# Kernel optimization log

Hardware: AMD Instinct MI355X
Metric: run time of the kernel (lower is better)

## Reference

```python
import jax, jax.numpy as jnp
import numpy as np
from jax import lax

DIM = 512; HEADS = 8; HD = DIM // HEADS; SM = 16; NS = 3
B = 8; HH = 32; WW = 32; N = HH * WW; HL = DIM // 4


def setup_inputs() -> dict:
    key = jax.random.key(0)
    ks = iter(jax.random.split(key, 64))
    def g(shape, s=0.02):
        return jax.random.normal(next(ks), shape, dtype=jnp.float32) * s
    z = lambda *sh: jnp.zeros(sh, jnp.float32)
    inp = {
        'x': jax.random.normal(next(ks), (B, N, DIM), dtype=jnp.float32),
        'H': HH, 'W': WW,
        'qkv_w': g((NS, 3 * DIM, DIM)),
        'proj_w': g((DIM, DIM)), 'proj_b': z(DIM),
        'pos_sw': g((HEADS, SM, HD, 2)), 'neg_sw': g((HEADS, SM, HD, 2)),
        'spec_mix': jnp.ones((HEADS, SM), jnp.float32),
        'ca_w1': g((DIM // 2, DIM)), 'ca_b1': z(DIM // 2),
        'ca_w2': g((HEADS * 4, DIM // 2)), 'ca_b2': z(HEADS * 4),
        'lstm_wih_f': g((4 * HL, DIM)), 'lstm_whh_f': g((4 * HL, HL)),
        'lstm_bih_f': z(4 * HL), 'lstm_bhh_f': z(4 * HL),
        'lstm_wih_b': g((4 * HL, DIM)), 'lstm_whh_b': g((4 * HL, HL)),
        'lstm_bih_b': z(4 * HL), 'lstm_bhh_b': z(4 * HL),
        'mha_in_w': g((3 * DIM, DIM)), 'mha_in_b': z(3 * DIM),
        'mha_out_w': g((DIM, DIM)), 'mha_out_b': z(DIM),
        'ge_w1': g((DIM // 2, DIM)), 'ge_b1': z(DIM // 2),
        'ge_w2': g((HEADS * 2, DIM // 2)), 'ge_b2': z(HEADS * 2),
        'spw': jnp.ones((NS, HEADS, HD), jnp.float32),
        'dwc_w5': g((HD, 1, 5, 5), 0.05), 'dwc_b5': z(HD),
        'dwc_w7': g((HD, 1, 7, 7), 0.05), 'dwc_b7': z(HD),
        'dwc_w9': g((HD, 1, 9, 9), 0.05), 'dwc_b9': z(HD),
        'mode_w': jnp.ones((3,), jnp.float32) / 3.0,
    }
    return inp


def reference(x, H, W, qkv_w, proj_w, proj_b, pos_sw, neg_sw, spec_mix,
              ca_w1, ca_b1, ca_w2, ca_b2,
              lstm_wih_f, lstm_whh_f, lstm_bih_f, lstm_bhh_f,
              lstm_wih_b, lstm_whh_b, lstm_bih_b, lstm_bhh_b,
              mha_in_w, mha_in_b, mha_out_w, mha_out_b,
              ge_w1, ge_b1, ge_w2, ge_b2, spw,
              dwc_w5, dwc_b5, dwc_w7, dwc_b7, dwc_w9, dwc_b9, mode_w):
    Bn, Nn, C = x.shape
    heads = HEADS; hd = C // heads

    # ---------- DynamicContextEncoder ----------
    def lstm_dir(xs, wih, whh, bih, bhh):
        # xs: (N, B, C); PyTorch gate order i,f,g,o
        gates_x = xs @ wih.T + (bih + bhh)
        hdim = whh.shape[1]
        def step(carry, gx):
            h, c = carry
            gi = gx + h @ whh.T
            i, f, gg, o = jnp.split(gi, 4, axis=-1)
            c = jax.nn.sigmoid(f) * c + jax.nn.sigmoid(i) * jnp.tanh(gg)
            h = jax.nn.sigmoid(o) * jnp.tanh(c)
            return (h, c), h
        z0 = jnp.zeros((xs.shape[1], hdim), xs.dtype)
        _, hs = lax.scan(step, (z0, z0), gates_x)
        return hs

    xs = jnp.swapaxes(x, 0, 1)  # (N, B, C)
    h_f = lstm_dir(xs, lstm_wih_f, lstm_whh_f, lstm_bih_f, lstm_bhh_f)
    h_b = lstm_dir(xs[::-1], lstm_wih_b, lstm_whh_b, lstm_bih_b, lstm_bhh_b)[::-1]
    local_ctx = jnp.concatenate([h_f, h_b], -1).mean(0)  # (B, dim//2)
    local_ctx = jnp.pad(local_ctx, ((0, 0), (0, C - local_ctx.shape[1])))

    nh2 = heads // 2; hd2 = C // nh2
    qkv_c = x @ mha_in_w.T + mha_in_b
    qc, kc, vc = jnp.split(qkv_c, 3, -1)
    sh = lambda t: t.reshape(Bn, Nn, nh2, hd2).transpose(0, 2, 1, 3)
    qc, kc, vc = sh(qc), sh(kc), sh(vc)
    attn = jax.nn.softmax(jnp.einsum('bhnd,bhmd->bhnm', qc, kc) / float(np.sqrt(hd2)), -1)
    ac = jnp.einsum('bhnm,bhmd->bhnd', attn, vc).transpose(0, 2, 1, 3).reshape(Bn, Nn, C)
    ac = ac @ mha_out_w.T + mha_out_b
    combined = x.mean(1) + local_ctx + ac.mean(1)
    coeffs = jax.nn.sigmoid(jax.nn.relu(combined @ ca_w1.T + ca_b1) @ ca_w2.T + ca_b2)
    coeffs = coeffs.reshape(Bn, heads, 4)

    # ---------- GradientInformedMixer coefficients (x_grad is zeros) ----------
    gz = jnp.zeros((Bn, C), x.dtype)
    gmix = jax.nn.softmax((jnp.tanh(gz @ ge_w1.T + ge_b1) @ ge_w2.T + ge_b2).reshape(Bn, heads, 2), -1)

    # ---------- SpectralPolarityMixer ----------
    smix = jax.nn.softmax(spec_mix, -1).mean(-1)[None, :, None, None]  # per-head scalar
    wp = (pos_sw[..., 0] + 1j * pos_sw[..., 1])[:, :SM, :SM]
    wn = (neg_sw[..., 0] + 1j * neg_sw[..., 1])[:, :SM, :SM]

    def spectral(t):
        tf = jnp.fft.rfft2(t)[:, :, :SM, :SM]
        tp = jnp.fft.irfft2(tf * wp[None], s=(Nn, hd))
        tn = jnp.fft.irfft2(tf * wn[None], s=(Nn, hd))
        return tp + tn * smix

    def safe_pow(t, p):  # relu(t)**p with safe grads
        tp = jnp.where(t > 0, t, 1.0)
        return jnp.where(t > 0, tp ** p, 0.0)

    mw = jax.nn.softmax(mode_w, 0)
    def dwc(xi, w, b):
        return lax.conv_general_dilated(xi, w, (1, 1), 'SAME',
                                        feature_group_count=xi.shape[1],
                                        dimension_numbers=('NCHW', 'OIHW', 'NCHW')) + b[None, :, None, None]

    c0, c1, c2, c3 = [coeffs[:, :, i][:, :, None, None] for i in range(4)]
    g0, g1 = gmix[:, :, 0][:, :, None, None], gmix[:, :, 1][:, :, None, None]

    outs = []
    for s in range(NS):
        qkv = (x @ qkv_w[s].T).reshape(Bn, Nn, 3, heads, hd).transpose(2, 0, 3, 1, 4)
        q, k, v = qkv[0], qkv[1], qkv[2]  # (B, heads, N, hd)
        q = spectral(q); k = spectral(k)
        p = (1.0 + jnp.abs(spw[s]))[None, :, None, :]
        q_pos = safe_pow(q, p); q_neg = safe_pow(-q, p)
        k_pos = safe_pow(k, p); k_neg = safe_pow(-k, p)
        kvpp = jnp.einsum('bhnd,bhne->bhde', k_pos, v)
        kvnn = jnp.einsum('bhnd,bhne->bhde', k_neg, v)
        z = (jnp.einsum('bhnd,bhd->bhn', q_pos, k_pos.sum(2))
             + jnp.einsum('bhnd,bhd->bhn', q_neg, k_neg.sum(2)) + 1e-6)[..., None]
        same = (c0 * jnp.einsum('bhnd,bhde->bhne', q_pos, kvpp)
                + c1 * jnp.einsum('bhnd,bhde->bhne', q_neg, kvnn)) / z
        opp = (c2 * jnp.einsum('bhnd,bhde->bhne', q_pos, kvnn)
               + c3 * jnp.einsum('bhnd,bhde->bhne', q_neg, kvpp)) / z
        mixed = g0 * same + g1 * opp
        v_img = v.reshape(Bn * heads, H, W, hd).transpose(0, 3, 1, 2)
        vcv = mw[0] * dwc(v_img, dwc_w5, dwc_b5) + mw[1] * dwc(v_img, dwc_w7, dwc_b7) + mw[2] * dwc(v_img, dwc_w9, dwc_b9)
        vcv = vcv.transpose(0, 2, 3, 1).reshape(Bn, heads, Nn, hd)
        outs.append(mixed + vcv)

    out = jnp.stack(outs).mean(0).transpose(0, 2, 1, 3).reshape(Bn, Nn, C)
    return out @ proj_w.T + proj_b
```

## Files before the change

kernel.cpp:

```cpp
#include <hip/hip_runtime.h>
#include <hip/hip_bf16.h>
#include <math.h>

typedef __bf16 bf16x8 __attribute__((ext_vector_type(8)));
typedef __bf16 bf16x4 __attribute__((ext_vector_type(4)));
typedef float  f32x4  __attribute__((ext_vector_type(4)));
typedef const float __attribute__((address_space(1)))* gf1p;

#define MFMA(a,b,c) __builtin_amdgcn_mfma_f32_16x16x32_bf16(a, b, c, 0, 0, 0)
#define LOG2E 1.4426950408889634f

static constexpr size_t OFF_R0    = 0;
static constexpr size_t OFF_GXT   = 12582912;
static constexpr size_t OFF_ACCUM = OFF_GXT;
static constexpr size_t OFF_FINAL = OFF_GXT + 4194304;
static constexpr size_t SOFF      = OFF_GXT + 8388608;
static constexpr size_t OFF_ROWSUM= SOFF;
static constexpr size_t OFF_ACMP  = OFF_ROWSUM;
static constexpr size_t OFF_COLW  = OFF_ROWSUM + 32768;
static constexpr size_t OFF_BM    = OFF_COLW;
static constexpr size_t OFF_XPART = OFF_COLW + 327680;
static constexpr size_t OFF_ACM   = OFF_COLW + 524288;
static constexpr size_t OFF_XMEAN = OFF_ACM + 4096;
static constexpr size_t OFF_LC    = OFF_XMEAN + 4096;
static constexpr size_t OFF_COEF  = OFF_LC + 2048;
static constexpr size_t OFF_GMIX  = OFF_COEF + 256;
static constexpr size_t OFF_MW    = OFF_GMIX + 16;
static constexpr size_t OFF_CONV9 = OFF_MW + 4;
static constexpr size_t OFF_CBIAS = OFF_CONV9 + 5184;
static constexpr size_t OFF_WEFF  = OFF_CBIAS + 64;
static constexpr size_t OFF_PPOW  = OFF_WEFF + 4096;
static constexpr size_t OFF_LBIAS = OFF_PPOW + 1536;
static constexpr size_t OFF_W2    = OFF_LBIAS + 1024;
static constexpr size_t OFF_W1CS  = OFF_W2 + 2048;
static constexpr size_t OFF_W1T   = OFF_W1CS + 16384;
static constexpr size_t OFF_XB    = OFF_FINAL;
static constexpr size_t OFF_QW    = OFF_FINAL + 2097152;
static constexpr size_t OFF_MW2   = OFF_FINAL + 3276800;
static constexpr size_t OFF_WFB   = OFF_FINAL + 3670016;
static constexpr size_t OFF_WBB   = OFF_FINAL + 3801088;
static constexpr size_t OFF_PWB   = OFF_FINAL + 3932160;

__device__ __forceinline__ float sigm(float x){ return __builtin_amdgcn_rcpf(1.0f + exp2f(-LOG2E*x)); }
__device__ __forceinline__ float tanhx(float x){ return 2.0f*__builtin_amdgcn_rcpf(1.0f + exp2f(-2.0f*LOG2E*x)) - 1.0f; }
__device__ __forceinline__ unsigned pk2(float a, float b){
  union { __bf16 h[2]; unsigned u; } z; z.h[0]=(__bf16)a; z.h[1]=(__bf16)b; return z.u;
}
__device__ __forceinline__ unsigned pk2b(__bf16 a, __bf16 b){
  union { __bf16 h[2]; unsigned u; } z; z.h[0]=a; z.h[1]=b; return z.u;
}
__device__ __forceinline__ void powpair(float t, float p, float& pos, float& neg){
  float a = fabsf(t);
  float v = (a > 0.f) ? exp2f(p * __log2f(a)) : 0.f;
  pos = (t > 0.f) ? v : 0.f;
  neg = (t < 0.f) ? v : 0.f;
}
__device__ __forceinline__ f32x4 fz4(){ return (f32x4){0.f,0.f,0.f,0.f}; }

__global__ void k_cvt_all(const float* __restrict__ x, const float* __restrict__ qkv_w,
                          const float* __restrict__ mha_in_w, const float* __restrict__ wih_f,
                          const float* __restrict__ wih_b, const float* __restrict__ proj_w,
                          float* __restrict__ ws){
  int b = blockIdx.x;
  const float* src; __bf16* dst; int base;
  if (b < 2048){      src=x;        dst=(__bf16*)(ws+OFF_XB);  base=b; }
  else if (b < 3200){ src=qkv_w;    dst=(__bf16*)(ws+OFF_QW);  base=b-2048; }
  else if (b < 3584){ src=mha_in_w; dst=(__bf16*)(ws+OFF_MW2); base=b-3200; }
  else if (b < 3712){ src=wih_f;    dst=(__bf16*)(ws+OFF_WFB); base=b-3584; }
  else if (b < 3840){ src=wih_b;    dst=(__bf16*)(ws+OFF_WBB); base=b-3712; }
  else {              src=proj_w;   dst=(__bf16*)(ws+OFF_PWB); base=b-3840; }
  int i = (base*256 + threadIdx.x)*8;
  f32x4 u0 = *(const f32x4*)(src+i), u1 = *(const f32x4*)(src+i+4);
  bf16x8 v;
  #pragma unroll
  for (int j=0;j<4;++j){ v[j]=(__bf16)u0[j]; v[j+4]=(__bf16)u1[j]; }
  *(bf16x8*)(dst+i) = v;
}

__global__ void k_const(const float* __restrict__ ge_b1, const float* __restrict__ ge_w2,
                        const float* __restrict__ ge_b2, const float* __restrict__ mode_w,
                        const float* __restrict__ w5, const float* __restrict__ b5,
                        const float* __restrict__ w7, const float* __restrict__ b7,
                        const float* __restrict__ w9, const float* __restrict__ b9,
                        const float* __restrict__ pos_sw, const float* __restrict__ neg_sw,
                        const float* __restrict__ spw,
                        const float* __restrict__ bih_f, const float* __restrict__ bhh_f,
                        const float* __restrict__ bih_b, const float* __restrict__ bhh_b,
                        float* __restrict__ ws){
  int tid = threadIdx.x;
  __shared__ float mw[3];
  __shared__ float tgh[256];
  __shared__ float sbuf[16];
  tgh[tid] = tanhf(ge_b1[tid]);
  if (tid == 0){
    float m0=mode_w[0], m1=mode_w[1], m2=mode_w[2];
    float mx = fmaxf(m0, fmaxf(m1,m2));
    float e0=expf(m0-mx), e1=expf(m1-mx), e2=expf(m2-mx);
    float s = e0+e1+e2;
    mw[0]=e0/s; mw[1]=e1/s; mw[2]=e2/s;
    ws[OFF_MW+0]=mw[0]; ws[OFF_MW+1]=mw[1]; ws[OFF_MW+2]=mw[2];
  }
  __syncthreads();
  if (tid < 16){
    float s = ge_b2[tid];
    for (int i=0;i<256;++i) s += ge_w2[tid*256+i]*tgh[i];
    sbuf[tid] = s;
  }
  __syncthreads();
  if (tid < 8){
    float a = sbuf[2*tid], b = sbuf[2*tid+1];
    float m = fmaxf(a,b);
    float ea = expf(a-m), eb = expf(b-m);
    ws[OFF_GMIX+2*tid]   = ea/(ea+eb);
    ws[OFF_GMIX+2*tid+1] = eb/(ea+eb);
  }
  for (int j=tid;j<512;j+=256){
    ws[OFF_LBIAS+j]     = bih_f[j]+bhh_f[j];
    ws[OFF_LBIAS+512+j] = bih_b[j]+bhh_b[j];
  }
  for (int f=tid; f<5184; f+=256){
    int d=f/81, t=f%81, ky=t/9, kx=t%9, dy=ky-4, dx=kx-4;
    float v = mw[2]*w9[d*81+t];
    if (dy>=-3 && dy<=3 && dx>=-3 && dx<=3) v += mw[1]*w7[d*49 + (dy+3)*7 + (dx+3)];
    if (dy>=-2 && dy<=2 && dx>=-2 && dx<=2) v += mw[0]*w5[d*25 + (dy+2)*5 + (dx+2)];
    ws[OFF_CONV9+f] = v;
  }
  if (tid<64) ws[OFF_CBIAS+tid] = mw[0]*b5[tid]+mw[1]*b7[tid]+mw[2]*b9[tid];
  for (int f=tid; f<2048; f+=256){
    int h=f>>8, k1=(f>>4)&15, k2=f&15;
    int src = ((h*16+k1)*64 + k2)*2;
    ws[OFF_WEFF+2*f]   = pos_sw[src]   + 0.0625f*neg_sw[src];
    ws[OFF_WEFF+2*f+1] = pos_sw[src+1] + 0.0625f*neg_sw[src+1];
  }
  for (int f=tid; f<1536; f+=256) ws[OFF_PPOW+f] = 1.0f + fabsf(spw[f]);
  for (int f=tid; f<1024; f+=256){
    int e=f>>4, k2=f&15; int ph=(e*k2)&63;
    float th = (float)ph * (6.283185307179586f/64.0f);
    ws[OFF_W2+2*f]   = cosf(th);
    ws[OFF_W2+2*f+1] = -sinf(th);
  }
  __bf16* w1cs = (__bf16*)(ws + OFF_W1CS);
  for (int f=tid; f<32768; f+=256){
    int r=f>>10, m=f&1023; int k1=r&15; int ph=(k1*m)&1023;
    float th = (float)ph * (6.283185307179586f/1024.0f);
    w1cs[f] = (__bf16)((r<16)?cosf(th):-sinf(th));
  }
  __bf16* w1t = (__bf16*)(ws + OFF_W1T);
  for (int f=tid; f<32768; f+=256){
    int n=f>>5, r=f&31; int k1=r&15; int ph=(k1*n)&1023;
    float th = (float)ph * (6.283185307179586f/1024.0f);
    w1t[f] = (__bf16)((r<16)?cosf(th):sinf(th));
  }
}

template<typename CT>
__global__ __launch_bounds__(256,2) void k_gemm_bf(const __bf16* __restrict__ A, const __bf16* __restrict__ W,
                                                   const float* __restrict__ bias, CT* __restrict__ C,
                                                   int NB_N, int N, int K){
  __shared__ __bf16 As[128][40];
  __shared__ __bf16 Ws[128][40];
  int tid = threadIdx.x;
  int nwg = gridDim.x, o = blockIdx.x;
  int cpx = nwg >> 3;
  int wg = (o & 7)*cpx + (o >> 3);
  int n0 = (wg % NB_N) * 128, m0 = (wg / NB_N) * 128;
  int l = tid & 63, wid = tid >> 6, lr = l & 15, lg = l >> 4;
  int wr = wid >> 1, wc = wid & 1;
  f32x4 acc[4][4];
  #pragma unroll
  for (int i=0;i<4;++i){ acc[i][0]=fz4(); acc[i][1]=fz4(); acc[i][2]=fz4(); acc[i][3]=fz4(); }
  int srow = tid >> 1, sk = (tid & 1) * 16;
  const __bf16* Ap = A + (size_t)(m0 + srow) * K + sk;
  const __bf16* Wp = W + (size_t)(n0 + srow) * K + sk;
  for (int k0 = 0; k0 < K; k0 += 32){
    bf16x8 a0 = *(const bf16x8*)(Ap), a1 = *(const bf16x8*)(Ap+8);
    bf16x8 w0 = *(const bf16x8*)(Wp), w1 = *(const bf16x8*)(Wp+8);
    Ap += 32; Wp += 32;
    __syncthreads();
    *(bf16x8*)&As[srow][sk]   = a0;  *(bf16x8*)&As[srow][sk+8] = a1;
    *(bf16x8*)&Ws[srow][sk]   = w0;  *(bf16x8*)&Ws[srow][sk+8] = w1;
    __syncthreads();
    bf16x8 aF[4], bF[4];
    #pragma unroll
    for (int mf=0;mf<4;++mf) aF[mf] = *(const bf16x8*)&As[wr*64+mf*16+lr][lg*8];
    #pragma unroll
    for (int nf=0;nf<4;++nf) bF[nf] = *(const bf16x8*)&Ws[wc*64+nf*16+lr][lg*8];
    #pragma unroll
    for (int mf=0;mf<4;++mf)
      #pragma unroll
      for (int nf=0;nf<4;++nf) acc[mf][nf] = MFMA(aF[mf], bF[nf], acc[mf][nf]);
  }
  #pragma unroll
  for (int mf=0;mf<4;++mf)
    #pragma unroll
    for (int nf=0;nf<4;++nf){
      int row = m0 + wr*64 + mf*16 + lg*4;
      int col = n0 + wc*64 + nf*16 + lr;
      float bv = bias ? bias[col] : 0.f;
      #pragma unroll
      for (int r=0;r<4;++r) C[(size_t)(row+r)*N + col] = (CT)(acc[mf][nf][r] + bv);
    }
}

__global__ __launch_bounds__(256,2) void k_gemm_acc(const float* __restrict__ accum, const __bf16* __restrict__ W,
                                                    const float* __restrict__ bias, float* __restrict__ C){
  const int N = 512, K = 512, NB_N = 4;
  __shared__ __bf16 As[128][40];
  __shared__ __bf16 Ws[128][40];
  int tid = threadIdx.x;
  int nwg = gridDim.x, o = blockIdx.x;
  int cpx = nwg >> 3;
  int wg = (o & 7)*cpx + (o >> 3);
  int n0 = (wg % NB_N) * 128, m0 = (wg / NB_N) * 128;
  int l = tid & 63, wid = tid >> 6, lr = l & 15, lg = l >> 4;
  int wr = wid >> 1, wc = wid & 1;
  f32x4 acc[4][4];
  #pragma unroll
  for (int i=0;i<4;++i){ acc[i][0]=fz4(); acc[i][1]=fz4(); acc[i][2]=fz4(); acc[i][3]=fz4(); }
  int srow = tid >> 1, sk = (tid & 1) * 16;
  int row = m0 + srow;
  int bb = row >> 10, nn = row & 1023;
  const float* Abase = accum + ((size_t)bb*8192 + nn)*64;
  const __bf16* Wp = W + (size_t)(n0 + srow) * K + sk;
  const float s3 = 1.0f/3.0f;
  for (int k0 = 0; k0 < K; k0 += 32){
    int c0 = k0 + sk;
    const float* Ap = Abase + (size_t)(c0>>6)*65536 + (c0&63);
    f32x4 a0=*(const f32x4*)(Ap), a1=*(const f32x4*)(Ap+4), a2=*(const f32x4*)(Ap+8), a3=*(const f32x4*)(Ap+12);
    bf16x8 w0 = *(const bf16x8*)(Wp), w1 = *(const bf16x8*)(Wp+8);
    Wp += 32;
    __syncthreads();
    bf16x8 va, vb;
    #pragma unroll
    for (int j=0;j<4;++j){ va[j]=(__bf16)(a0[j]*s3); va[j+4]=(__bf16)(a1[j]*s3);
                           vb[j]=(__bf16)(a2[j]*s3); vb[j+4]=(__bf16)(a3[j]*s3); }
    *(bf16x8*)&As[srow][sk]   = va;  *(bf16x8*)&As[srow][sk+8] = vb;
    *(bf16x8*)&Ws[srow][sk]   = w0;  *(bf16x8*)&Ws[srow][sk+8] = w1;
    __syncthreads();
    bf16x8 aF[4], bF[4];
    #pragma unroll
    for (int mf=0;mf<4;++mf) aF[mf] = *(const bf16x8*)&As[wr*64+mf*16+lr][lg*8];
    #pragma unroll
    for (int nf=0;nf<4;++nf) bF[nf] = *(const bf16x8*)&Ws[wc*64+nf*16+lr][lg*8];
    #pragma unroll
    for (int mf=0;mf<4;++mf)
      #pragma unroll
      for (int nf=0;nf<4;++nf) acc[mf][nf] = MFMA(aF[mf], bF[nf], acc[mf][nf]);
  }
  #pragma unroll
  for (int mf=0;mf<4;++mf)
    #pragma unroll
    for (int nf=0;nf<4;++nf){
      int orow = m0 + wr*64 + mf*16 + lg*4;
      int col = n0 + wc*64 + nf*16 + lr;
      float bv = bias[col];
      #pragma unroll
      for (int r=0;r<4;++r) C[(size_t)(orow+r)*N + col] = acc[mf][nf][r] + bv;
    }
}

__global__ __launch_bounds__(256,1) void k_lstm_scan(const float* __restrict__ whh_f,
                                                     const float* __restrict__ whh_b,
                                                     const float* __restrict__ gates,
                                                     float* __restrict__ lc){
  int dir = blockIdx.x >> 3, b = blockIdx.x & 7;
  const float* __restrict__ whh = dir ? whh_b : whh_f;
  const float* gx0 = gates + (size_t)b*1048576;
  gf1p gx1 = (gf1p)(unsigned long long)gx0;
  int tid=threadIdx.x, w=tid>>6, l=tid&63;
  int lr=l&15, lg=l>>4;
  bf16x8 wf[4][2][4];
  #pragma unroll
  for (int q=0;q<4;++q)
    #pragma unroll
    for (int t=0;t<2;++t)
      #pragma unroll
      for (int kc=0;kc<4;++kc){
        const float* p = whh + (size_t)(q*128 + w*32 + t*16 + lr)*128 + kc*32 + lg*8;
        bf16x8 v;
        #pragma unroll
        for (int j=0;j<8;++j) v[j]=(__bf16)p[j];
        wf[q][t][kc]=v;
      }
  __shared__ __bf16 hbuf[2][132];
  for (int i=tid; i<264; i+=256) ((__bf16*)hbuf)[i] = (__bf16)0.0f;
  int tsel = l&1, rsel = (l>>1)&3;
  int hrow = w*32 + tsel*16 + lg*4 + rsel;
  long toff = (dir ? (long)1023*1024 : 0) + dir*512 + hrow;
  long tstride = dir ? -1024 : 1024;
  float cs=0.f, hs=0.f;
  float g0[4], g1[4], g2[4], g3[4];
  #pragma unroll
  for (int q=0;q<4;++q) g0[q] = gx1[toff + q*128];
  toff += tstride;
  #pragma unroll
  for (int q=0;q<4;++q) g1[q] = gx1[toff + q*128];
  toff += tstride;
  #pragma unroll
  for (int q=0;q<4;++q) g2[q] = gx1[toff + q*128];
  toff += tstride;
  #pragma unroll
  for (int q=0;q<4;++q) g3[q] = gx1[toff + q*128];
  toff += tstride;
  __syncthreads();

#define LSTM_STEP(RB, WB, G) { \
    float gq[4]; \
    _Pragma("unroll") for (int q=0;q<4;++q) gq[q]=G[q]; \
    _Pragma("unroll") for (int q=0;q<4;++q) G[q] = gx1[toff + q*128]; \
    toff += tstride; \
    if (toff < 0) toff = 0;   \
    bf16x8 hf[4]; \
    _Pragma("unroll") for (int kc=0;kc<4;++kc) hf[kc] = *(const bf16x8*)&hbuf[RB][kc*32 + lg*8]; \
    f32x4 acc[4][2]; \
    _Pragma("unroll") for (int q=0;q<4;++q){ acc[q][0]=fz4(); acc[q][1]=fz4(); } \
    _Pragma("unroll") for (int kc=0;kc<4;++kc) \
      _Pragma("unroll") for (int q=0;q<4;++q){ \
        acc[q][0] = MFMA(wf[q][0][kc], hf[kc], acc[q][0]); \
        acc[q][1] = MFMA(wf[q][1][kc], hf[kc], acc[q][1]); } \
    float gv[4]; \
    _Pragma("unroll") for (int q=0;q<4;++q){ \
      f32x4 v0 = acc[q][0], v1 = acc[q][1]; \
      float a01 = (rsel&1) ? v0[1] : v0[0]; \
      float a23 = (rsel&1) ? v0[3] : v0[2]; \
      float av  = (rsel&2) ? a23 : a01; \
      float b01 = (rsel&1) ? v1[1] : v1[0]; \
      float b23 = (rsel&1) ? v1[3] : v1[2]; \
      float bv  = (rsel&2) ? b23 : b01; \
      gv[q] = (tsel ? bv : av) + gq[q]; } \
    float ii=sigm(gv[0]), ff=sigm(gv[1]), gg=tanhx(gv[2]), oo=sigm(gv[3]); \
    cs = ff*cs + ii*gg; \
    float hv = oo*tanhx(cs); \
    hs += hv; \
    if (!(l&8)) hbuf[WB][hrow] = (__bf16)hv; \
    asm volatile("s_waitcnt lgkmcnt(0)" ::: "memory"); \
    __builtin_amdgcn_sched_barrier(0); \
    __builtin_amdgcn_s_barrier(); \
    __builtin_amdgcn_sched_barrier(0); }

  for (int it=0; it<256; ++it){
    LSTM_STEP(0, 1, g0)
    LSTM_STEP(1, 0, g1)
    LSTM_STEP(0, 1, g2)
    LSTM_STEP(1, 0, g3)
  }
#undef LSTM_STEP
  if (!(l&8)) lc[b*256 + dir*128 + hrow] = hs*(1.f/1024.f);
}

template<int MODE>
__global__ __launch_bounds__(256,1) void k_mha(const __bf16* __restrict__ qkv, float* __restrict__ rowsum,
                                               float* __restrict__ colw){
  int rb = blockIdx.x, h2 = blockIdx.y, b = blockIdx.z;
  __shared__ __bf16 Qs[256][136];
  __shared__ __bf16 Ks[128][136];
  int tid=threadIdx.x, l=tid&63, w=tid>>6, lr=l&15, lg=l>>4;
  {
    const float qs = LOG2E / sqrtf(128.0f);
    int row = tid;
    const __bf16* p = qkv + ((size_t)(b*1024 + rb*256 + row))*1536 + h2*128;
    #pragma unroll
    for (int cc=0; cc<128; cc+=8){
      bf16x8 u = *(const bf16x8*)(p+cc);
      bf16x8 v;
      #pragma unroll
      for (int j=0;j<8;++j) v[j]=(__bf16)((float)u[j]*qs);
      *(bf16x8*)&Qs[row][cc] = v;
    }
  }
  float rs[4][4];
  if (MODE==1){
    #pragma unroll
    for (int mf=0;mf<4;++mf){ rs[mf][0]=0.f; rs[mf][1]=0.f; rs[mf][2]=0.f; rs[mf][3]=0.f; }
  } else {
    #pragma unroll
    for (int mf=0;mf<4;++mf)
      #pragma unroll
      for (int r=0;r<4;++r)
        rs[mf][r] = 1.0f / rowsum[((size_t)(b*4+h2))*1024 + rb*256 + w*64 + mf*16 + lg*4 + r];
  }
  for (int mc=0; mc<8; ++mc){
    __syncthreads();
    {
      int row = tid>>1, co = (tid&1)*64;
      const __bf16* p = qkv + ((size_t)(b*1024 + mc*128 + row))*1536 + 512 + h2*128 + co;
      #pragma unroll
      for (int cc=0; cc<64; cc+=8)
        *(bf16x8*)&Ks[row][co+cc] = *(const bf16x8*)(p+cc);
    }
    __syncthreads();
    f32x4 acc[4][8];
    #pragma unroll
    for (int mf=0;mf<4;++mf)
      #pragma unroll
      for (int nf=0;nf<8;++nf) acc[mf][nf]=fz4();
    #pragma unroll
    for (int ks=0;ks<4;++ks){
      bf16x8 aF[4], bFv[8];
      #pragma unroll
      for (int mf=0;mf<4;++mf) aF[mf] = *(const bf16x8*)&Qs[w*64+mf*16+lr][ks*32+lg*8];
      #pragma unroll
      for (int nf=0;nf<8;++nf) bFv[nf] = *(const bf16x8*)&Ks[nf*16+lr][ks*32+lg*8];
      #pragma unroll
      for (int mf=0;mf<4;++mf)
        #pragma unroll
        for (int nf=0;nf<8;++nf) acc[mf][nf] = MFMA(aF[mf], bFv[nf], acc[mf][nf]);
    }
    if (MODE==1){
      #pragma unroll
      for (int mf=0;mf<4;++mf)
        #pragma unroll
        for (int nf=0;nf<8;++nf)
          #pragma unroll
          for (int r=0;r<4;++r) rs[mf][r] += exp2f(acc[mf][nf][r]);
    } else {
      #pragma unroll
      for (int nf=0;nf<8;++nf){
        float cv = 0.f;
        #pragma unroll
        for (int mf=0;mf<4;++mf)
          #pragma unroll
          for (int r=0;r<4;++r) cv += exp2f(acc[mf][nf][r])*rs[mf][r];
        cv += __shfl_xor(cv,16);
        cv += __shfl_xor(cv,32);
        if (lg==0)
          colw[(((size_t)(rb*4+w)*8 + b)*4 + h2)*1024 + mc*128 + nf*16 + lr] = cv;
      }
    }
  }
  if (MODE==1){
    #pragma unroll
    for (int mf=0;mf<4;++mf)
      #pragma unroll
      for (int r=0;r<4;++r){
        float v = rs[mf][r];
        v += __shfl_xor(v,1); v += __shfl_xor(v,2); v += __shfl_xor(v,4); v += __shfl_xor(v,8);
        if (lr==0) rowsum[((size_t)(b*4+h2))*1024 + rb*256 + w*64 + mf*16 + lg*4 + r] = v;
      }
  }
}

__global__ void k_mha3(const __bf16* __restrict__ qkv, const float* __restrict__ colw, float* __restrict__ acmp){
  int h2 = blockIdx.x, b = blockIdx.y, ms = blockIdx.z;
  int tid = threadIdx.x;
  __shared__ float cwred[128];
  if (tid < 128){
    float cw=0.f;
    #pragma unroll
    for (int t16=0;t16<16;++t16) cw += colw[(((size_t)t16*8 + b)*4 + h2)*1024 + ms*128 + tid];
    cwred[tid]=cw;
  }
  __syncthreads();
  int e = tid & 127, half = tid >> 7;
  float s = 0.f;
  for (int ml = half*64; ml < half*64+64; ++ml)
    s += cwred[ml] * (float)qkv[((size_t)(b*1024 + ms*128 + ml))*1536 + 1024 + h2*128 + e];
  __shared__ float red[256];
  red[tid]=s; __syncthreads();
  if (tid<128) acmp[((size_t)(ms*8+b))*512 + h2*128 + e] = red[tid]+red[tid+128];
}

__global__ void k_xmean1(const float* __restrict__ x, float* __restrict__ xpart){
  int sl = blockIdx.x, b = blockIdx.y;
  int tid = threadIdx.x;
  #pragma unroll
  for (int cc=0; cc<2; ++cc){
    int c = tid + cc*256;
    float s=0.f;
    for (int n=sl*64; n<sl*64+64; ++n) s += x[((size_t)(b*1024+n))*512 + c];
    xpart[((size_t)(b*16+sl))*512 + c] = s;
  }
}

__global__ __launch_bounds__(256) void k_coeffs(float* __restrict__ ws,
                        const float* __restrict__ mow, const float* __restrict__ mob,
                        const float* __restrict__ ca_w1, const float* __restrict__ ca_b1,
                        const float* __restrict__ ca_w2, const float* __restrict__ ca_b2){
  int b = blockIdx.x, tid = threadIdx.x;
  __shared__ float av[512], comb[512], hid[256];
  for (int i=tid;i<512;i+=256){
    float s = 0.f;
    #pragma unroll
    for (int ms=0; ms<8; ++ms) s += ws[OFF_ACMP + ((size_t)(ms*8+b))*512 + i];
    av[i] = s*(1.f/1024.f);
  }
  __syncthreads();
  for (int c=tid;c<512;c+=256){
    float s = mob[c];
    for (int k=0;k<512;++k) s += mow[(size_t)c*512+k]*av[k];
    float xm = 0.f;
    #pragma unroll
    for (int sl=0; sl<16; ++sl) xm += ws[OFF_XPART + ((size_t)(b*16+sl))*512 + c];
    comb[c] = s + xm*(1.f/1024.f) + ((c<256) ? ws[OFF_LC + b*256 + c] : 0.f);
  }
  __syncthreads();
  for (int j=tid;j<256;j+=256){
    float s = ca_b1[j];
    for (int k=0;k<512;++k) s += ca_w1[(size_t)j*512+k]*comb[k];
    hid[j] = fmaxf(s,0.f);
  }
  __syncthreads();
  if (tid<32){
    float s = ca_b2[tid];
    for (int k=0;k<256;++k) s += ca_w2[tid*256+k]*hid[k];
    ws[OFF_COEF + b*32 + tid] = 1.f/(1.f+expf(-s));
  }
}

__global__ __launch_bounds__(256,2) void k_spec(__bf16* __restrict__ qkv, const float* __restrict__ ws){
  int qk = blockIdx.x, h = blockIdx.y, b = blockIdx.z;
  int colbase = qk*512 + h*64;
  int tid=threadIdx.x, l=tid&63, w=tid>>6, lr=l&15, lg=l>>4;
  __shared__ __bf16 tT[64][520];
  __shared__ float M1[32][64];
  __shared__ float G2[256][2];
  __shared__ __bf16 hbl[2048];
  const __bf16* w1cs = (const __bf16*)(ws + OFF_W1CS);
  f32x4 acc1[2]; acc1[0]=fz4(); acc1[1]=fz4();
  for (int c0=0; c0<2; ++c0){
    __syncthreads();
    {
      int p = tid;
      int m0 = c0*512 + 2*p;
      const __bf16* r0 = qkv + ((size_t)(b*1024 + m0))*1536 + colbase;
      const __bf16* r1 = r0 + 1536;
      #pragma unroll
      for (int e=0;e<64;e+=8){
        bf16x8 u0 = *(const bf16x8*)(r0+e);
        bf16x8 u1 = *(const bf16x8*)(r1+e);
        #pragma unroll
        for (int j=0;j<8;++j) *(unsigned*)&tT[e+j][2*p] = pk2b(u0[j], u1[j]);
      }
    }
    __syncthreads();
    for (int ks=0; ks<16; ++ks){
      bf16x8 bfv = *(const bf16x8*)&tT[w*16+lr][ks*32+lg*8];
      #pragma unroll
      for (int mf=0;mf<2;++mf){
        bf16x8 af = *(const bf16x8*)(w1cs + (size_t)(mf*16+lr)*1024 + c0*512 + ks*32 + lg*8);
        acc1[mf] = MFMA(af, bfv, acc1[mf]);
      }
    }
  }
  #pragma unroll
  for (int mf=0;mf<2;++mf)
    #pragma unroll
    for (int r=0;r<4;++r) M1[mf*16 + lg*4 + r][w*16 + lr] = acc1[mf][r];
  __syncthreads();
  {
    int k1 = tid>>4, k2 = tid&15;
    float tfr=0.f, tfi=0.f;
    const float* w2 = ws + OFF_W2;
    for (int e=0;e<64;++e){
      float mr = M1[k1][e], mi = M1[16+k1][e];
      float cr = w2[(e*16+k2)*2], ci = w2[(e*16+k2)*2+1];
      tfr += mr*cr - mi*ci;
      tfi += mr*ci + mi*cr;
    }
    float wr = ws[OFF_WEFF + ((size_t)h*256 + k1*16 + k2)*2];
    float wi = ws[OFF_WEFF + ((size_t)h*256 + k1*16 + k2)*2 + 1];
    G2[tid][0] = tfr*wr - tfi*wi;
    G2[tid][1] = tfr*wi + tfi*wr;
  }
  __syncthreads();
  {
    const float* w2 = ws + OFF_W2;
    for (int f=tid; f<1024; f+=256){
      int k1 = f>>6, d = f&63;
      float hr=0.f, hi=0.f;
      #pragma unroll
      for (int k2=0;k2<16;++k2){
        float gr=G2[k1*16+k2][0], gi=G2[k1*16+k2][1];
        float sc = k2 ? 2.f : 1.f;
        float cr = sc*w2[(d*16+k2)*2];
        float ci = -sc*w2[(d*16+k2)*2+1];
        hr += gr*cr - gi*ci;
        hi += gr*ci + gi*cr;
      }
      const float inv = 1.0f/65536.0f;
      hbl[d*32 + k1]      = (__bf16)(hr*inv);
      hbl[d*32 + 16 + k1] = (__bf16)(-hi*inv);
    }
  }
  __syncthreads();
  const __bf16* w1t = (const __bf16*)(ws + OFF_W1T);
  bf16x8 bF[4];
  #pragma unroll
  for (int nf=0;nf<4;++nf) bF[nf] = *(const bf16x8*)&hbl[(nf*16+lr)*32 + lg*8];
  for (int pass=0; pass<4; ++pass){
    int rowbase = w*256 + pass*64;
    f32x4 acc[4][4];
    #pragma unroll
    for (int mf=0;mf<4;++mf){ acc[mf][0]=fz4(); acc[mf][1]=fz4(); acc[mf][2]=fz4(); acc[mf][3]=fz4(); }
    #pragma unroll
    for (int mf=0;mf<4;++mf){
      bf16x8 aF = *(const bf16x8*)(w1t + (size_t)(rowbase+mf*16+lr)*32 + lg*8);
      #pragma unroll
      for (int nf=0;nf<4;++nf) acc[mf][nf] = MFMA(aF, bF[nf], acc[mf][nf]);
    }
    #pragma unroll
    for (int mf=0;mf<4;++mf)
      #pragma unroll
      for (int nf=0;nf<4;++nf)
        #pragma unroll
        for (int r=0;r<4;++r){
          int n = rowbase + mf*16 + lg*4 + r;
          int d = nf*16 + lr;
          qkv[((size_t)(b*1024+n))*1536 + colbase + d] = (__bf16)acc[mf][nf][r];
        }
  }
}

__global__ __launch_bounds__(256,2) void k_polar_kv(const __bf16* __restrict__ qkv, float* __restrict__ ws,
                                                    int s){
  int h = blockIdx.x, b = blockIdx.y;
  int tid=threadIdx.x, l=tid&63, w=tid>>6, lr=l&15, lg=l>>4;
  __shared__ float plds[14300];
  __bf16* kpT = (__bf16*)plds;
  __bf16* knT = (__bf16*)((char*)plds + 17408);
  __bf16* vT  = (__bf16*)((char*)plds + 34816);
  float* scal = (float*)((char*)plds + 56576);
  float* pvs  = scal + 8;
  if (tid<4)  scal[tid] = ws[OFF_COEF + b*32 + h*4 + tid];
  if (tid==4) scal[4] = ws[OFF_GMIX + 2*h];
  if (tid==5) scal[5] = ws[OFF_GMIX + 2*h+1];
  if (tid<64) pvs[tid] = ws[OFF_PPOW + ((size_t)s*8+h)*64 + tid];
  for (int i=tid; i<16*136; i+=256) vT[64*136 + i] = (__bf16)((i<136)?1.0f:0.0f);
  f32x4 acc[4][5];
  #pragma unroll
  for (int mf=0;mf<4;++mf)
    #pragma unroll
    for (int nf=0;nf<5;++nf) acc[mf][nf]=fz4();
  for (int mc=0;mc<8;++mc){
    __syncthreads();
    #pragma unroll
    for (int it=0; it<16; ++it){
      int flat = tid + 256*it;
      int d = flat & 63, np = flat >> 6;
      int n = mc*128 + 2*np;
      const __bf16* kr = qkv + ((size_t)(b*1024+n))*1536 + 512 + h*64 + d;
      const __bf16* vr = qkv + ((size_t)(b*1024+n))*1536 + 1024 + h*64 + d;
      float p = pvs[d];
      float k0=(float)kr[0], k1=(float)kr[1536];
      float kp0,kn0,kp1,kn1;
      powpair(k0,p,kp0,kn0); powpair(k1,p,kp1,kn1);
      *(unsigned*)&kpT[d*136 + 2*np] = pk2(kp0,kp1);
      *(unsigned*)&knT[d*136 + 2*np] = pk2(kn0,kn1);
      *(unsigned*)&vT [d*136 + 2*np] = pk2b(vr[0], vr[1536]);
    }
    __syncthreads();
    const __bf16* A = (w&2)?knT:kpT;
    int kh = (w&1)*64;
    #pragma unroll
    for (int ks=0;ks<2;++ks){
      bf16x8 aF[4];
      #pragma unroll
      for (int mf=0;mf<4;++mf) aF[mf] = *(const bf16x8*)&A[(mf*16+lr)*136 + kh + ks*32 + lg*8];
      #pragma unroll
      for (int nf=0;nf<5;++nf){
        bf16x8 bFv = *(const bf16x8*)&vT[(nf*16+lr)*136 + kh + ks*32 + lg*8];
        #pragma unroll
        for (int mf=0;mf<4;++mf) acc[mf][nf] = MFMA(aF[mf], bFv, acc[mf][nf]);
      }
    }
  }
  __syncthreads();
  float* kvf = plds;
  if ((w&1)==0){
    int mat = w>>1;
    #pragma unroll
    for (int mf=0;mf<4;++mf)
      #pragma unroll
      for (int nf=0;nf<5;++nf)
        #pragma unroll
        for (int r=0;r<4;++r)
          kvf[((size_t)mat*64 + mf*16+lg*4+r)*80 + nf*16+lr] = acc[mf][nf][r];
  }
  __syncthreads();
  if (w&1){
    int mat = w>>1;
    #pragma unroll
    for (int mf=0;mf<4;++mf)
      #pragma unroll
      for (int nf=0;nf<5;++nf)
        #pragma unroll
        for (int r=0;r<4;++r)
          kvf[((size_t)mat*64 + mf*16+lg*4+r)*80 + nf*16+lr] += acc[mf][nf][r];
  }
  __syncthreads();
  __bf16* bmg = (__bf16*)(ws + OFF_BM) + (size_t)(b*8+h)*10240;
  {
    float c0=scal[0], c1=scal[1], c2=scal[2], c3=scal[3], g0=scal[4], g1=scal[5];
    for (int f=tid; f<80*128; f+=256){
      int e=f>>7, kk=f&127;
      float v;
      if (e<64){
        if (kk<64) v = g0*c0*kvf[kk*80+e] + g1*c2*kvf[(64+kk)*80+e];
        else { int k2=kk-64; v = g0*c1*kvf[(64+k2)*80+e] + g1*c3*kvf[k2*80+e]; }
      } else if (e==64){
        v = (kk<64) ? kvf[kk*80+64] : kvf[(64+(kk-64))*80+64];
      } else v = 0.f;
      bmg[f] = (__bf16)v;
    }
  }
}

__global__ __launch_bounds__(256,2) void k_polar_ap(const __bf16* __restrict__ qkv, const float* __restrict__ ws,
                                                    float* __restrict__ accum, int s){
  int pass8 = blockIdx.x, h = blockIdx.y, b = blockIdx.z;
  int tid=threadIdx.x, l=tid&63, w=tid>>6, lr=l&15, lg=l>>4;
  __shared__ __bf16 At[128*136];
  __shared__ __bf16 BmL[80*136];
  __shared__ float zb[128];
  __shared__ float pvs[64];
  if (tid<64) pvs[tid] = ws[OFF_PPOW + ((size_t)s*8+h)*64 + tid];
  {
    const __bf16* bmg = (const __bf16*)(ws + OFF_BM) + (size_t)(b*8+h)*10240;
    for (int u=tid; u<80*16; u+=256){
      int e=u>>4, kx=(u&15)*8;
      *(bf16x8*)&BmL[e*136+kx] = *(const bf16x8*)(bmg + e*128 + kx);
    }
  }
  __syncthreads();
  #pragma unroll
  for (int it=0; it<8; ++it){
    int flat = tid + 256*it;
    int row = flat>>4, dg = flat&15;
    int n = pass8*128 + row;
    const __bf16* qr = qkv + ((size_t)(b*1024+n))*1536 + h*64 + dg*4;
    bf16x4 u = *(const bf16x4*)qr;
    float qp[4], qn[4];
    #pragma unroll
    for (int j=0;j<4;++j) powpair((float)u[j], pvs[dg*4+j], qp[j], qn[j]);
    *(unsigned*)&At[row*136 + dg*4]        = pk2(qp[0],qp[1]);
    *(unsigned*)&At[row*136 + dg*4+2]      = pk2(qp[2],qp[3]);
    *(unsigned*)&At[row*136 + 64 + dg*4]   = pk2(qn[0],qn[1]);
    *(unsigned*)&At[row*136 + 64 + dg*4+2] = pk2(qn[2],qn[3]);
  }
  __syncthreads();
  f32x4 a2[2][5];
  #pragma unroll
  for (int mf=0;mf<2;++mf)
    #pragma unroll
    for (int nf=0;nf<5;++nf) a2[mf][nf]=fz4();
  #pragma unroll
  for (int ks=0;ks<4;++ks){
    bf16x8 aF[2];
    #pragma unroll
    for (int mf=0;mf<2;++mf) aF[mf] = *(const bf16x8*)&At[(w*32+mf*16+lr)*136 + ks*32 + lg*8];
    #pragma unroll
    for (int nf=0;nf<5;++nf){
      bf16x8 bFv = *(const bf16x8*)&BmL[(nf*16+lr)*136 + ks*32 + lg*8];
      #pragma unroll
      for (int mf=0;mf<2;++mf) a2[mf][nf] = MFMA(aF[mf], bFv, a2[mf][nf]);
    }
  }
  if (lr==0){
    #pragma unroll
    for (int mf=0;mf<2;++mf)
      #pragma unroll
      for (int r=0;r<4;++r) zb[w*32 + mf*16 + lg*4 + r] = a2[mf][4][r] + 1e-6f;
  }
  __syncthreads();
  #pragma unroll
  for (int mf=0;mf<2;++mf){
    float rz[4];
    #pragma unroll
    for (int r=0;r<4;++r) rz[r] = 1.0f / zb[w*32 + mf*16 + lg*4 + r];
    #pragma unroll
    for (int nf=0;nf<4;++nf)
      #pragma unroll
      for (int r=0;r<4;++r){
        int n = pass8*128 + w*32 + mf*16 + lg*4 + r;
        int e = nf*16 + lr;
        size_t oi = ((size_t)((b*8+h)*1024) + n)*64 + e;
        float v = a2[mf][nf][r]*rz[r];
        if (s==0) accum[oi] = v; else accum[oi] += v;
      }
  }
}

__global__ __launch_bounds__(256,2) void k_conv(const __bf16* __restrict__ qkv, const float* __restrict__ ws,
                                                float* __restrict__ accum){
  int bid = blockIdx.x;
  int sl = bid & 3, h = (bid>>2)&7, b = bid>>5;
  int tid = threadIdx.x;
  __shared__ float vs[1024][16];
  __shared__ float wc[16][81];
  __shared__ float cb[16];
  #pragma unroll
  for (int it=0; it<8; ++it){
    int flat = tid + 256*it;
    int pix = flat>>1, cg = (flat&1)*8;
    bf16x8 u = *(const bf16x8*)(qkv + ((size_t)(b*1024+pix))*1536 + 1024 + h*64 + sl*16 + cg);
    #pragma unroll
    for (int j=0;j<8;++j) vs[pix][cg+j] = (float)u[j];
  }
  for (int f=tid; f<16*81; f+=256) wc[f/81][f%81] = ws[OFF_CONV9 + (size_t)(sl*16 + f/81)*81 + (f%81)];
  if (tid<16) cb[tid] = ws[OFF_CBIAS + sl*16 + tid];
  __syncthreads();
  #pragma unroll
  for (int cc=0; cc<2; ++cc){
    int col = tid + 256*cc;
    int c = col & 15, x = col >> 4;
    float a[32];
    #pragma unroll
    for (int y=0;y<32;++y) a[y]=0.f;
    #pragma unroll
    for (int dx=-4; dx<=4; ++dx){
      int xx = x+dx;
      bool xv = (xx>=0)&&(xx<32);
      float colv[40];
      #pragma unroll
      for (int i=0;i<40;++i){
        int yy = i-4;
        colv[i] = (xv && yy>=0 && yy<32) ? vs[yy*32+xx][c] : 0.f;
      }
      #pragma unroll
      for (int dy=0; dy<9; ++dy){
        float wv = wc[c][dy*9 + dx+4];
        #pragma unroll
        for (int y=0;y<32;++y) a[y] += wv*colv[y+dy];
      }
    }
    float bias = cb[c];
    #pragma unroll
    for (int y=0;y<32;++y){
      size_t oi = ((size_t)((b*8+h)*1024) + y*32 + x)*64 + sl*16 + c;
      accum[oi] += a[y] + bias;
    }
  }
}

extern "C" void kernel_launch(void* const* d_in, const int* in_sizes, int n_in,
                              void* d_out, int out_size, void* d_ws, size_t ws_size,
                              hipStream_t stream){
  const float* x        = (const float*)d_in[0];
  const float* qkv_w    = (const float*)d_in[3];
  const float* proj_w   = (const float*)d_in[4];
  const float* proj_b   = (const float*)d_in[5];
  const float* pos_sw   = (const float*)d_in[6];
  const float* neg_sw   = (const float*)d_in[7];
  const float* ca_w1    = (const float*)d_in[9];
  const float* ca_b1    = (const float*)d_in[10];
  const float* ca_w2    = (const float*)d_in[11];
  const float* ca_b2    = (const float*)d_in[12];
  const float* wih_f    = (const float*)d_in[13];
  const float* whh_f    = (const float*)d_in[14];
  const float* bih_f    = (const float*)d_in[15];
  const float* bhh_f    = (const float*)d_in[16];
  const float* wih_b    = (const float*)d_in[17];
  const float* whh_b    = (const float*)d_in[18];
  const float* bih_b    = (const float*)d_in[19];
  const float* bhh_b    = (const float*)d_in[20];
  const float* mha_in_w = (const float*)d_in[21];
  const float* mha_in_b = (const float*)d_in[22];
  const float* mha_out_w= (const float*)d_in[23];
  const float* mha_out_b= (const float*)d_in[24];
  const float* ge_b1    = (const float*)d_in[26];
  const float* ge_w2    = (const float*)d_in[27];
  const float* ge_b2    = (const float*)d_in[28];
  const float* spw      = (const float*)d_in[29];
  const float* w5 = (const float*)d_in[30]; const float* b5 = (const float*)d_in[31];
  const float* w7 = (const float*)d_in[32]; const float* b7 = (const float*)d_in[33];
  const float* w9 = (const float*)d_in[34]; const float* b9 = (const float*)d_in[35];
  const float* mode_w = (const float*)d_in[36];
  float* ws  = (float*)d_ws;
  float* out = (float*)d_out;
  __bf16* xb   = (__bf16*)(ws + OFF_XB);
  __bf16* qwb  = (__bf16*)(ws + OFF_QW);
  __bf16* mwb  = (__bf16*)(ws + OFF_MW2);
  __bf16* wfb  = (__bf16*)(ws + OFF_WFB);
  __bf16* pwb  = (__bf16*)(ws + OFF_PWB);
  __bf16* qkvb = (__bf16*)(ws + OFF_R0);

  k_const<<<1,256,0,stream>>>(ge_b1, ge_w2, ge_b2, mode_w, w5,b5,w7,b7,w9,b9,
                              pos_sw, neg_sw, spw, bih_f,bhh_f,bih_b,bhh_b, ws);
  k_cvt_all<<<3968,256,0,stream>>>(x, qkv_w, mha_in_w, wih_f, wih_b, proj_w, ws);
  k_gemm_bf<float><<<512,256,0,stream>>>(xb, wfb, ws+OFF_LBIAS, ws+OFF_R0, 8, 1024, 512);
  k_lstm_scan<<<16,256,0,stream>>>(whh_f, whh_b, ws+OFF_R0, ws+OFF_LC);
  k_gemm_bf<__bf16><<<768,256,0,stream>>>(xb, mwb, mha_in_b, qkvb, 12, 1536, 512);
  k_mha<1><<<dim3(4,4,8),256,0,stream>>>(qkvb, ws+OFF_ROWSUM, ws+OFF_COLW);
  k_mha<2><<<dim3(4,4,8),256,0,stream>>>(qkvb, ws+OFF_ROWSUM, ws+OFF_COLW);
  k_mha3<<<dim3(4,8,8),256,0,stream>>>(qkvb, ws+OFF_COLW, ws+OFF_ACMP);
  k_xmean1<<<dim3(16,8),256,0,stream>>>(x, ws+OFF_XPART);
  k_coeffs<<<8,256,0,stream>>>(ws, mha_out_w, mha_out_b, ca_w1, ca_b1, ca_w2, ca_b2);
  for (int s=0; s<3; ++s){
    k_gemm_bf<__bf16><<<768,256,0,stream>>>(xb, qwb + (size_t)s*786432, nullptr, qkvb, 12, 1536, 512);
    k_spec<<<dim3(2,8,8),256,0,stream>>>(qkvb, ws);
    k_polar_kv<<<dim3(8,8),256,0,stream>>>(qkvb, ws, s);
    k_polar_ap<<<dim3(8,8,8),256,0,stream>>>(qkvb, ws, ws+OFF_ACCUM, s);
    k_conv<<<256,256,0,stream>>>(qkvb, ws, ws+OFF_ACCUM);
  }
  k_gemm_acc<<<256,256,0,stream>>>(ws+OFF_ACCUM, pwb, proj_b, out);
}
```

Before: 1.384 ms.

## Overlap LSTM scan with MHA GEMM and scale work via fused mega-kernels

Splits the serial LSTM scan into two phases with state saved in workspace, and runs each phase inside heterogeneous mega-kernels alongside the MHA in-projection GEMM, x-mean, spectral and conv work for the first scale. This lets the latency-bound 16-block recurrence overlap with otherwise independent work. LSTM gate precomputation is now stored as bf16 in the output buffer instead of fp32, and a second qkv buffer lets MHA and scale paths coexist. Conv now initializes the accumulator, so the polar kernel always adds. The cost is more complex scheduling, lower gate precision, and occupancy capped at one block per CU in the mega-kernels.

After: 1.402 ms (median of 2 runs). About the same (+1.3%).

```diff
diff --git a/kernel.cpp b/kernel.cpp
--- a/kernel.cpp
+++ b/kernel.cpp
@@ -5,7 +5,6 @@
 typedef __bf16 bf16x8 __attribute__((ext_vector_type(8)));
 typedef __bf16 bf16x4 __attribute__((ext_vector_type(4)));
 typedef float  f32x4  __attribute__((ext_vector_type(4)));
-typedef const float __attribute__((address_space(1)))* gf1p;
 
 #define MFMA(a,b,c) __builtin_amdgcn_mfma_f32_16x16x32_bf16(a, b, c, 0, 0, 0)
 #define LOG2E 1.4426950408889634f
@@ -19,7 +18,6 @@
 static constexpr size_t OFF_ACMP  = OFF_ROWSUM;
 static constexpr size_t OFF_COLW  = OFF_ROWSUM + 32768;
 static constexpr size_t OFF_BM    = OFF_COLW;
-static constexpr size_t OFF_XPART = OFF_COLW + 327680;
 static constexpr size_t OFF_ACM   = OFF_COLW + 524288;
 static constexpr size_t OFF_XMEAN = OFF_ACM + 4096;
 static constexpr size_t OFF_LC    = OFF_XMEAN + 4096;
@@ -34,6 +32,9 @@
 static constexpr size_t OFF_W2    = OFF_LBIAS + 1024;
 static constexpr size_t OFF_W1CS  = OFF_W2 + 2048;
 static constexpr size_t OFF_W1T   = OFF_W1CS + 16384;
+static constexpr size_t OFF_HB    = OFF_W1T + 16384;
+static constexpr size_t OFF_STATE = OFF_HB;
+static constexpr size_t OFF_XP2   = OFF_HB + 16384;
 static constexpr size_t OFF_XB    = OFF_FINAL;
 static constexpr size_t OFF_QW    = OFF_FINAL + 2097152;
 static constexpr size_t OFF_MW2   = OFF_FINAL + 3276800;
@@ -153,14 +154,12 @@
   }
 }
 
-template<typename CT>
-__global__ __launch_bounds__(256,2) void k_gemm_bf(const __bf16* __restrict__ A, const __bf16* __restrict__ W,
-                                                   const float* __restrict__ bias, CT* __restrict__ C,
-                                                   int NB_N, int N, int K){
-  __shared__ __bf16 As[128][40];
-  __shared__ __bf16 Ws[128][40];
-  int tid = threadIdx.x;
-  int nwg = gridDim.x, o = blockIdx.x;
+
+__device__ __forceinline__ void d_gemm(const __bf16* __restrict__ A, const __bf16* __restrict__ W,
+                                       const float* __restrict__ bias, __bf16* __restrict__ C,
+                                       int NB_N, int N, int K, int o, int nwg, int tid, char* smraw){
+  __bf16 (*As)[40] = (__bf16(*)[40])smraw;
+  __bf16 (*Ws)[40] = (__bf16(*)[40])(smraw + 10240);
   int cpx = nwg >> 3;
   int wg = (o & 7)*cpx + (o >> 3);
   int n0 = (wg % NB_N) * 128, m0 = (wg / NB_N) * 128;
@@ -198,77 +197,18 @@
       int col = n0 + wc*64 + nf*16 + lr;
       float bv = bias ? bias[col] : 0.f;
       #pragma unroll
-      for (int r=0;r<4;++r) C[(size_t)(row+r)*N + col] = (CT)(acc[mf][nf][r] + bv);
-    }
-}
-
-__global__ __launch_bounds__(256,2) void k_gemm_acc(const float* __restrict__ accum, const __bf16* __restrict__ W,
-                                                    const float* __restrict__ bias, float* __restrict__ C){
-  const int N = 512, K = 512, NB_N = 4;
-  __shared__ __bf16 As[128][40];
-  __shared__ __bf16 Ws[128][40];
-  int tid = threadIdx.x;
-  int nwg = gridDim.x, o = blockIdx.x;
-  int cpx = nwg >> 3;
-  int wg = (o & 7)*cpx + (o >> 3);
-  int n0 = (wg % NB_N) * 128, m0 = (wg / NB_N) * 128;
-  int l = tid & 63, wid = tid >> 6, lr = l & 15, lg = l >> 4;
-  int wr = wid >> 1, wc = wid & 1;
-  f32x4 acc[4][4];
-  #pragma unroll
-  for (int i=0;i<4;++i){ acc[i][0]=fz4(); acc[i][1]=fz4(); acc[i][2]=fz4(); acc[i][3]=fz4(); }
-  int srow = tid >> 1, sk = (tid & 1) * 16;
-  int row = m0 + srow;
-  int bb = row >> 10, nn = row & 1023;
-  const float* Abase = accum + ((size_t)bb*8192 + nn)*64;
-  const __bf16* Wp = W + (size_t)(n0 + srow) * K + sk;
-  const float s3 = 1.0f/3.0f;
-  for (int k0 = 0; k0 < K; k0 += 32){
-    int c0 = k0 + sk;
-    const float* Ap = Abase + (size_t)(c0>>6)*65536 + (c0&63);
-    f32x4 a0=*(const f32x4*)(Ap), a1=*(const f32x4*)(Ap+4), a2=*(const f32x4*)(Ap+8), a3=*(const f32x4*)(Ap+12);
-    bf16x8 w0 = *(const bf16x8*)(Wp), w1 = *(const bf16x8*)(Wp+8);
-    Wp += 32;
-    __syncthreads();
-    bf16x8 va, vb;
-    #pragma unroll
-    for (int j=0;j<4;++j){ va[j]=(__bf16)(a0[j]*s3); va[j+4]=(__bf16)(a1[j]*s3);
-                           vb[j]=(__bf16)(a2[j]*s3); vb[j+4]=(__bf16)(a3[j]*s3); }
-    *(bf16x8*)&As[srow][sk]   = va;  *(bf16x8*)&As[srow][sk+8] = vb;
-    *(bf16x8*)&Ws[srow][sk]   = w0;  *(bf16x8*)&Ws[srow][sk+8] = w1;
-    __syncthreads();
-    bf16x8 aF[4], bF[4];
-    #pragma unroll
-    for (int mf=0;mf<4;++mf) aF[mf] = *(const bf16x8*)&As[wr*64+mf*16+lr][lg*8];
-    #pragma unroll
-    for (int nf=0;nf<4;++nf) bF[nf] = *(const bf16x8*)&Ws[wc*64+nf*16+lr][lg*8];
-    #pragma unroll
-    for (int mf=0;mf<4;++mf)
-      #pragma unroll
-      for (int nf=0;nf<4;++nf) acc[mf][nf] = MFMA(aF[mf], bF[nf], acc[mf][nf]);
-  }
-  #pragma unroll
-  for (int mf=0;mf<4;++mf)
-    #pragma unroll
-    for (int nf=0;nf<4;++nf){
-      int orow = m0 + wr*64 + mf*16 + lg*4;
-      int col = n0 + wc*64 + nf*16 + lr;
-      float bv = bias[col];
-      #pragma unroll
-      for (int r=0;r<4;++r) C[(size_t)(orow+r)*N + col] = acc[mf][nf][r] + bv;
-    }
-}
-
-__global__ __launch_bounds__(256,1) void k_lstm_scan(const float* __restrict__ whh_f,
-                                                     const float* __restrict__ whh_b,
-                                                     const float* __restrict__ gates,
-                                                     float* __restrict__ lc){
-  int dir = blockIdx.x >> 3, b = blockIdx.x & 7;
+      for (int r=0;r<4;++r) C[(size_t)(row+r)*N + col] = (__bf16)(acc[mf][nf][r] + bv);
+    }
+}
+
+template<int PHASE>
+__device__ __forceinline__ void d_lstm(const float* __restrict__ whh_f, const float* __restrict__ whh_b,
+                                       const __bf16* __restrict__ gates, float* __restrict__ lc,
+                                       float* __restrict__ state, int bid, int tid, char* smraw){
+  int dir = bid >> 3, b = bid & 7;
   const float* __restrict__ whh = dir ? whh_b : whh_f;
-  const float* gx0 = gates + (size_t)b*1048576;
-  gf1p gx1 = (gf1p)(unsigned long long)gx0;
-  int tid=threadIdx.x, w=tid>>6, l=tid&63;
-  int lr=l&15, lg=l>>4;
+  const __bf16* gx = gates + (size_t)b*1048576;
+  int w=tid>>6, l=tid&63, lr=l&15, lg=l>>4;
   bf16x8 wf[4][2][4];
   #pragma unroll
   for (int q=0;q<4;++q)
@@ -282,34 +222,43 @@
         for (int j=0;j<8;++j) v[j]=(__bf16)p[j];
         wf[q][t][kc]=v;
       }
-  __shared__ __bf16 hbuf[2][132];
-  for (int i=tid; i<264; i+=256) ((__bf16*)hbuf)[i] = (__bf16)0.0f;
+  __bf16 (*hbuf)[132] = (__bf16(*)[132])smraw;
   int tsel = l&1, rsel = (l>>1)&3;
   int hrow = w*32 + tsel*16 + lg*4 + rsel;
-  long toff = (dir ? (long)1023*1024 : 0) + dir*512 + hrow;
+  float* st = state + bid*768 + tid*3;
+  float cs, hs;
+  if (PHASE==0){
+    for (int i=tid; i<264; i+=256) ((__bf16*)hbuf)[i] = (__bf16)0.0f;
+    cs=0.f; hs=0.f;
+  } else {
+    cs = st[0]; hs = st[1];
+    hbuf[0][hrow] = (__bf16)st[2];
+  }
+  long t0 = (PHASE==0) ? (dir?1023:0) : (dir?511:512);
   long tstride = dir ? -1024 : 1024;
-  float cs=0.f, hs=0.f;
+  long toff = t0*1024 + dir*512 + hrow;
   float g0[4], g1[4], g2[4], g3[4];
   #pragma unroll
-  for (int q=0;q<4;++q) g0[q] = gx1[toff + q*128];
+  for (int q=0;q<4;++q) g0[q] = (float)gx[toff + q*128];
   toff += tstride;
   #pragma unroll
-  for (int q=0;q<4;++q) g1[q] = gx1[toff + q*128];
+  for (int q=0;q<4;++q) g1[q] = (float)gx[toff + q*128];
   toff += tstride;
   #pragma unroll
-  for (int q=0;q<4;++q) g2[q] = gx1[toff + q*128];
+  for (int q=0;q<4;++q) g2[q] = (float)gx[toff + q*128];
   toff += tstride;
   #pragma unroll
-  for (int q=0;q<4;++q) g3[q] = gx1[toff + q*128];
+  for (int q=0;q<4;++q) g3[q] = (float)gx[toff + q*128];
   toff += tstride;
   __syncthreads();
 
 #define LSTM_STEP(RB, WB, G) { \
     float gq[4]; \
     _Pragma("unroll") for (int q=0;q<4;++q) gq[q]=G[q]; \
-    _Pragma("unroll") for (int q=0;q<4;++q) G[q] = gx1[toff + q*128]; \
+    _Pragma("unroll") for (int q=0;q<4;++q) G[q] = (float)gx[toff + q*128]; \
     toff += tstride; \
-    if (toff < 0) toff = 0;   \
+    if (toff < 0) toff = 0; \
+    if (toff > 1048000) toff = 1048000; \
     bf16x8 hf[4]; \
     _Pragma("unroll") for (int kc=0;kc<4;++kc) hf[kc] = *(const bf16x8*)&hbuf[RB][kc*32 + lg*8]; \
     f32x4 acc[4][2]; \
@@ -338,23 +287,39 @@
     __builtin_amdgcn_s_barrier(); \
     __builtin_amdgcn_sched_barrier(0); }
 
-  for (int it=0; it<256; ++it){
+  for (int it=0; it<128; ++it){
     LSTM_STEP(0, 1, g0)
     LSTM_STEP(1, 0, g1)
     LSTM_STEP(0, 1, g2)
     LSTM_STEP(1, 0, g3)
   }
 #undef LSTM_STEP
-  if (!(l&8)) lc[b*256 + dir*128 + hrow] = hs*(1.f/1024.f);
+  if (PHASE==0){
+    st[0]=cs; st[1]=hs; st[2]=(float)hbuf[0][hrow];
+  } else {
+    if (!(l&8)) lc[b*256 + dir*128 + hrow] = hs*(1.f/1024.f);
+  }
+}
+
+__device__ __forceinline__ void d_xmean(const float* __restrict__ x, float* __restrict__ xpart,
+                                        int f, int tid){
+  int sl = f & 15, b = f >> 4;
+  #pragma unroll
+  for (int cc=0; cc<2; ++cc){
+    int c = tid + cc*256;
+    float s=0.f;
+    for (int n=sl*64; n<sl*64+64; ++n) s += x[((size_t)(b*1024+n))*512 + c];
+    xpart[((size_t)(b*16+sl))*512 + c] = s;
+  }
 }
 
 template<int MODE>
-__global__ __launch_bounds__(256,1) void k_mha(const __bf16* __restrict__ qkv, float* __restrict__ rowsum,
-                                               float* __restrict__ colw){
-  int rb = blockIdx.x, h2 = blockIdx.y, b = blockIdx.z;
-  __shared__ __bf16 Qs[256][136];
-  __shared__ __bf16 Ks[128][136];
-  int tid=threadIdx.x, l=tid&63, w=tid>>6, lr=l&15, lg=l>>4;
+__device__ __forceinline__ void d_mha(const __bf16* __restrict__ qkv, float* __restrict__ rowsum,
+                                      float* __restrict__ colw, int f, int tid, char* smraw){
+  int rb = f & 3, h2 = (f>>2) & 3, b = f >> 4;
+  __bf16 (*Qs)[136] = (__bf16(*)[136])smraw;
+  __bf16 (*Ks)[136] = (__bf16(*)[136])(smraw + 69632);
+  int l=tid&63, w=tid>>6, lr=l&15, lg=l>>4;
   {
     const float qs = LOG2E / sqrtf(128.0f);
     int row = tid;
@@ -440,81 +405,15 @@
   }
 }
 
-__global__ void k_mha3(const __bf16* __restrict__ qkv, const float* __restrict__ colw, float* __restrict__ acmp){
-  int h2 = blockIdx.x, b = blockIdx.y, ms = blockIdx.z;
-  int tid = threadIdx.x;
-  __shared__ float cwred[128];
-  if (tid < 128){
-    float cw=0.f;
-    #pragma unroll
-    for (int t16=0;t16<16;++t16) cw += colw[(((size_t)t16*8 + b)*4 + h2)*1024 + ms*128 + tid];
-    cwred[tid]=cw;
-  }
-  __syncthreads();
-  int e = tid & 127, half = tid >> 7;
-  float s = 0.f;
-  for (int ml = half*64; ml < half*64+64; ++ml)
-    s += cwred[ml] * (float)qkv[((size_t)(b*1024 + ms*128 + ml))*1536 + 1024 + h2*128 + e];
-  __shared__ float red[256];
-  red[tid]=s; __syncthreads();
-  if (tid<128) acmp[((size_t)(ms*8+b))*512 + h2*128 + e] = red[tid]+red[tid+128];
-}
-
-__global__ void k_xmean1(const float* __restrict__ x, float* __restrict__ xpart){
-  int sl = blockIdx.x, b = blockIdx.y;
-  int tid = threadIdx.x;
-  #pragma unroll
-  for (int cc=0; cc<2; ++cc){
-    int c = tid + cc*256;
-    float s=0.f;
-    for (int n=sl*64; n<sl*64+64; ++n) s += x[((size_t)(b*1024+n))*512 + c];
-    xpart[((size_t)(b*16+sl))*512 + c] = s;
-  }
-}
-
-__global__ __launch_bounds__(256) void k_coeffs(float* __restrict__ ws,
-                        const float* __restrict__ mow, const float* __restrict__ mob,
-                        const float* __restrict__ ca_w1, const float* __restrict__ ca_b1,
-                        const float* __restrict__ ca_w2, const float* __restrict__ ca_b2){
-  int b = blockIdx.x, tid = threadIdx.x;
-  __shared__ float av[512], comb[512], hid[256];
-  for (int i=tid;i<512;i+=256){
-    float s = 0.f;
-    #pragma unroll
-    for (int ms=0; ms<8; ++ms) s += ws[OFF_ACMP + ((size_t)(ms*8+b))*512 + i];
-    av[i] = s*(1.f/1024.f);
-  }
-  __syncthreads();
-  for (int c=tid;c<512;c+=256){
-    float s = mob[c];
-    for (int k=0;k<512;++k) s += mow[(size_t)c*512+k]*av[k];
-    float xm = 0.f;
-    #pragma unroll
-    for (int sl=0; sl<16; ++sl) xm += ws[OFF_XPART + ((size_t)(b*16+sl))*512 + c];
-    comb[c] = s + xm*(1.f/1024.f) + ((c<256) ? ws[OFF_LC + b*256 + c] : 0.f);
-  }
-  __syncthreads();
-  for (int j=tid;j<256;j+=256){
-    float s = ca_b1[j];
-    for (int k=0;k<512;++k) s += ca_w1[(size_t)j*512+k]*comb[k];
-    hid[j] = fmaxf(s,0.f);
-  }
-  __syncthreads();
-  if (tid<32){
-    float s = ca_b2[tid];
-    for (int k=0;k<256;++k) s += ca_w2[tid*256+k]*hid[k];
-    ws[OFF_COEF + b*32 + tid] = 1.f/(1.f+expf(-s));
-  }
-}
-
-__global__ __launch_bounds__(256,2) void k_spec(__bf16* __restrict__ qkv, const float* __restrict__ ws){
-  int qk = blockIdx.x, h = blockIdx.y, b = blockIdx.z;
+__device__ __forceinline__ void d_spec(__bf16* __restrict__ qkv, const float* __restrict__ ws,
+                                       int f, int tid, char* smraw){
+  int qk = f & 1, h = (f>>1) & 7, b = f >> 4;
   int colbase = qk*512 + h*64;
-  int tid=threadIdx.x, l=tid&63, w=tid>>6, lr=l&15, lg=l>>4;
-  __shared__ __bf16 tT[64][520];
-  __shared__ float M1[32][64];
-  __shared__ float G2[256][2];
-  __shared__ __bf16 hbl[2048];
+  int l=tid&63, w=tid>>6, lr=l&15, lg=l>>4;
+  __bf16 (*tT)[520] = (__bf16(*)[520])smraw;
+  float (*M1)[64]   = (float(*)[64])(smraw + 66560);
+  float (*G2)[2]    = (float(*)[2])(smraw + 66560 + 8192);
+  __bf16* hbl       = (__bf16*)(smraw + 66560 + 8192 + 2048);
   const __bf16* w1cs = (const __bf16*)(ws + OFF_W1CS);
   f32x4 acc1[2]; acc1[0]=fz4(); acc1[1]=fz4();
   for (int c0=0; c0<2; ++c0){
@@ -565,8 +464,8 @@
   __syncthreads();
   {
     const float* w2 = ws + OFF_W2;
-    for (int f=tid; f<1024; f+=256){
-      int k1 = f>>6, d = f&63;
+    for (int f2=tid; f2<1024; f2+=256){
+      int k1 = f2>>6, d = f2&63;
       float hr=0.f, hi=0.f;
       #pragma unroll
       for (int k2=0;k2<16;++k2){
@@ -608,6 +507,161 @@
           int d = nf*16 + lr;
           qkv[((size_t)(b*1024+n))*1536 + colbase + d] = (__bf16)acc[mf][nf][r];
         }
+  }
+}
+
+__device__ __forceinline__ void d_conv(const __bf16* __restrict__ qkv, const float* __restrict__ ws,
+                                       float* __restrict__ accum, int f, int tid, char* smraw, bool init){
+  int sl = f & 3, h = (f>>2)&7, b = f>>5;
+  float (*vs)[16] = (float(*)[16])smraw;
+  float (*wc)[81] = (float(*)[81])(smraw + 65536);
+  float* cb       = (float*)(smraw + 65536 + 5184);
+  #pragma unroll
+  for (int it=0; it<8; ++it){
+    int flat = tid + 256*it;
+    int pix = flat>>1, cg = (flat&1)*8;
+    bf16x8 u = *(const bf16x8*)(qkv + ((size_t)(b*1024+pix))*1536 + 1024 + h*64 + sl*16 + cg);
+    #pragma unroll
+    for (int j=0;j<8;++j) vs[pix][cg+j] = (float)u[j];
+  }
+  for (int f2=tid; f2<16*81; f2+=256) wc[f2/81][f2%81] = ws[OFF_CONV9 + (size_t)(sl*16 + f2/81)*81 + (f2%81)];
+  if (tid<16) cb[tid] = ws[OFF_CBIAS + sl*16 + tid];
+  __syncthreads();
+  #pragma unroll
+  for (int cc=0; cc<2; ++cc){
+    int col = tid + 256*cc;
+    int c = col & 15, x = col >> 4;
+    float a[32];
+    #pragma unroll
+    for (int y=0;y<32;++y) a[y]=0.f;
+    #pragma unroll
+    for (int dx=-4; dx<=4; ++dx){
+      int xx = x+dx;
+      bool xv = (xx>=0)&&(xx<32);
+      float colv[40];
+      #pragma unroll
+      for (int i=0;i<40;++i){
+        int yy = i-4;
+        colv[i] = (xv && yy>=0 && yy<32) ? vs[yy*32+xx][c] : 0.f;
+      }
+      #pragma unroll
+      for (int dy=0; dy<9; ++dy){
+        float wv = wc[c][dy*9 + dx+4];
+        #pragma unroll
+        for (int y=0;y<32;++y) a[y] += wv*colv[y+dy];
+      }
+    }
+    float bias = cb[c];
+    #pragma unroll
+    for (int y=0;y<32;++y){
+      size_t oi = ((size_t)((b*8+h)*1024) + y*32 + x)*64 + sl*16 + c;
+      if (init) accum[oi] = a[y] + bias;
+      else      accum[oi] += a[y] + bias;
+    }
+  }
+}
+
+
+__global__ __launch_bounds__(256,2) void k_gemm_bf(const __bf16* __restrict__ A, const __bf16* __restrict__ W,
+                                                   const float* __restrict__ bias, __bf16* __restrict__ C,
+                                                   int NB_N, int N, int K){
+  __shared__ __align__(16) char sm[20480];
+  d_gemm(A, W, bias, C, NB_N, N, K, blockIdx.x, gridDim.x, threadIdx.x, sm);
+}
+
+__global__ __launch_bounds__(256,1) void k_mega1(const float* __restrict__ whh_f, const float* __restrict__ whh_b,
+                                                 const __bf16* __restrict__ gates, float* __restrict__ ws,
+                                                 const float* __restrict__ x,
+                                                 const __bf16* __restrict__ xb, const __bf16* __restrict__ mwb,
+                                                 const float* __restrict__ mha_in_b, __bf16* __restrict__ qkvA){
+  __shared__ __align__(16) char sm[20480];
+  int bid = blockIdx.x, tid = threadIdx.x;
+  if (bid < 16)        d_lstm<0>(whh_f, whh_b, gates, ws+OFF_LC, ws+OFF_STATE, bid, tid, sm);
+  else if (bid < 784)  d_gemm(xb, mwb, mha_in_b, qkvA, 12, 1536, 512, bid-16, 768, tid, sm);
+  else                 d_xmean(x, ws+OFF_XP2, bid-784, tid);
+}
+
+__global__ __launch_bounds__(256,1) void k_mega2(const float* __restrict__ whh_f, const float* __restrict__ whh_b,
+                                                 const __bf16* __restrict__ gates, float* __restrict__ ws,
+                                                 const __bf16* __restrict__ qkvA, __bf16* __restrict__ qkvB,
+                                                 float* __restrict__ accum){
+  __shared__ __align__(16) char sm[104448];
+  int bid = blockIdx.x, tid = threadIdx.x;
+  if (bid < 16)        d_lstm<1>(whh_f, whh_b, gates, ws+OFF_LC, ws+OFF_STATE, bid, tid, sm);
+  else if (bid < 144)  d_spec(qkvB, ws, bid-16, tid, sm);
+  else if (bid < 272)  d_mha<1>(qkvA, ws+OFF_ROWSUM, ws+OFF_COLW, bid-144, tid, sm);
+  else                 d_conv(qkvA  == nullptr ? qkvA : qkvB, ws, accum, bid-272, tid, sm, true);
+}
+
+__global__ __launch_bounds__(256,1) void k_mha2_w(const __bf16* __restrict__ qkv, float* __restrict__ rowsum,
+                                                  float* __restrict__ colw){
+  __shared__ __align__(16) char sm[104448];
+  d_mha<2>(qkv, rowsum, colw, blockIdx.x, threadIdx.x, sm);
+}
+
+__global__ __launch_bounds__(256,2) void k_spec_w(__bf16* __restrict__ qkv, const float* __restrict__ ws){
+  __shared__ __align__(16) char sm[80896];
+  d_spec(qkv, ws, blockIdx.x, threadIdx.x, sm);
+}
+
+__global__ __launch_bounds__(256,2) void k_conv_w(const __bf16* __restrict__ qkv, const float* __restrict__ ws,
+                                                  float* __restrict__ accum){
+  __shared__ __align__(16) char sm[70784];
+  d_conv(qkv, ws, accum, blockIdx.x, threadIdx.x, sm, false);
+}
+
+__global__ void k_mha3(const __bf16* __restrict__ qkv, const float* __restrict__ colw, float* __restrict__ acmp){
+  int h2 = blockIdx.x, b = blockIdx.y, ms = blockIdx.z;
+  int tid = threadIdx.x;
+  __shared__ float cwred[128];
+  if (tid < 128){
+    float cw=0.f;
+    #pragma unroll
+    for (int t16=0;t16<16;++t16) cw += colw[(((size_t)t16*8 + b)*4 + h2)*1024 + ms*128 + tid];
+    cwred[tid]=cw;
+  }
+  __syncthreads();
+  int e = tid & 127, half = tid >> 7;
+  float s = 0.f;
+  for (int ml = half*64; ml < half*64+64; ++ml)
+    s += cwred[ml] * (float)qkv[((size_t)(b*1024 + ms*128 + ml))*1536 + 1024 + h2*128 + e];
+  __shared__ float red[256];
+  red[tid]=s; __syncthreads();
+  if (tid<128) acmp[((size_t)(ms*8+b))*512 + h2*128 + e] = red[tid]+red[tid+128];
+}
+
+__global__ __launch_bounds__(256) void k_coeffs(float* __restrict__ ws,
+                        const float* __restrict__ mow, const float* __restrict__ mob,
+                        const float* __restrict__ ca_w1, const float* __restrict__ ca_b1,
+                        const float* __restrict__ ca_w2, const float* __restrict__ ca_b2){
+  int b = blockIdx.x, tid = threadIdx.x;
+  __shared__ float av[512], comb[512], hid[256];
+  for (int i=tid;i<512;i+=256){
+    float s = 0.f;
+    #pragma unroll
+    for (int ms=0; ms<8; ++ms) s += ws[OFF_ACMP + ((size_t)(ms*8+b))*512 + i];
+    av[i] = s*(1.f/1024.f);
+  }
+  __syncthreads();
+  for (int c=tid;c<512;c+=256){
+    float s = mob[c];
+    for (int k=0;k<512;++k) s += mow[(size_t)c*512+k]*av[k];
+    float xm = 0.f;
+    #pragma unroll
+    for (int sl=0; sl<16; ++sl) xm += ws[OFF_XP2 + ((size_t)(b*16+sl))*512 + c];
+    comb[c] = s + xm*(1.f/1024.f) + ((c<256) ? ws[OFF_LC + b*256 + c] : 0.f);
+  }
+  __syncthreads();
+  for (int j=tid;j<256;j+=256){
+    float s = ca_b1[j];
+    for (int k=0;k<512;++k) s += ca_w1[(size_t)j*512+k]*comb[k];
+    hid[j] = fmaxf(s,0.f);
+  }
+  __syncthreads();
+  if (tid<32){
+    float s = ca_b2[tid];
+    for (int k=0;k<256;++k) s += ca_w2[tid*256+k]*hid[k];
+    ws[OFF_COEF + b*32 + tid] = 1.f/(1.f+expf(-s));
   }
 }
 
@@ -774,62 +828,66 @@
         int n = pass8*128 + w*32 + mf*16 + lg*4 + r;
         int e = nf*16 + lr;
         size_t oi = ((size_t)((b*8+h)*1024) + n)*64 + e;
-        float v = a2[mf][nf][r]*rz[r];
-        if (s==0) accum[oi] = v; else accum[oi] += v;
+        accum[oi] += a2[mf][nf][r]*rz[r];
       }
   }
 }
 
-__global__ __launch_bounds__(256,2) void k_conv(const __bf16* __restrict__ qkv, const float* __restrict__ ws,
-                                                float* __restrict__ accum){
-  int bid = blockIdx.x;
-  int sl = bid & 3, h = (bid>>2)&7, b = bid>>5;
+__global__ __launch_bounds__(256,2) void k_gemm_acc(const float* __restrict__ accum, const __bf16* __restrict__ W,
+                                                    const float* __restrict__ bias, float* __restrict__ C){
+  const int N = 512, K = 512, NB_N = 4;
+  __shared__ __bf16 As[128][40];
+  __shared__ __bf16 Ws[128][40];
   int tid = threadIdx.x;
-  __shared__ float vs[1024][16];
-  __shared__ float wc[16][81];
-  __shared__ float cb[16];
-  #pragma unroll
-  for (int it=0; it<8; ++it){
-    int flat = tid + 256*it;
-    int pix = flat>>1, cg = (flat&1)*8;
-    bf16x8 u = *(const bf16x8*)(qkv + ((size_t)(b*1024+pix))*1536 + 1024 + h*64 + sl*16 + cg);
-    #pragma unroll
-    for (int j=0;j<8;++j) vs[pix][cg+j] = (float)u[j];
-  }
-  for (int f=tid; f<16*81; f+=256) wc[f/81][f%81] = ws[OFF_CONV9 + (size_t)(sl*16 + f/81)*81 + (f%81)];
-  if (tid<16) cb[tid] = ws[OFF_CBIAS + sl*16 + tid];
-  __syncthreads();
-  #pragma unroll
-  for (int cc=0; cc<2; ++cc){
-    int col = tid + 256*cc;
-    int c = col & 15, x = col >> 4;
-    float a[32];
-    #pragma unroll
-    for (int y=0;y<32;++y) a[y]=0.f;
-    #pragma unroll
-    for (int dx=-4; dx<=4; ++dx){
-      int xx = x+dx;
-      bool xv = (xx>=0)&&(xx<32);
-      float colv[40];
-      #pragma unroll
-      for (int i=0;i<40;++i){
-        int yy = i-4;
-        colv[i] = (xv && yy>=0 && yy<32) ? vs[yy*32+xx][c] : 0.f;
-      }
-      #pragma unroll
-      for (int dy=0; dy<9; ++dy){
-        float wv = wc[c][dy*9 + dx+4];
-        #pragma unroll
-        for (int y=0;y<32;++y) a[y] += wv*colv[y+dy];
-      }
-    }
-    float bias = cb[c];
-    #pragma unroll
-    for (int y=0;y<32;++y){
-      size_t oi = ((size_t)((b*8+h)*1024) + y*32 + x)*64 + sl*16 + c;
-      accum[oi] += a[y] + bias;
-    }
-  }
+  int nwg = gridDim.x, o = blockIdx.x;
+  int cpx = nwg >> 3;
+  int wg = (o & 7)*cpx + (o >> 3);
+  int n0 = (wg % NB_N) * 128, m0 = (wg / NB_N) * 128;
+  int l = tid & 63, wid = tid >> 6, lr = l & 15, lg = l >> 4;
+  int wr = wid >> 1, wc = wid & 1;
+  f32x4 acc[4][4];
+  #pragma unroll
+  for (int i=0;i<4;++i){ acc[i][0]=fz4(); acc[i][1]=fz4(); acc[i][2]=fz4(); acc[i][3]=fz4(); }
+  int srow = tid >> 1, sk = (tid & 1) * 16;
+  int row = m0 + srow;
+  int bb = row >> 10, nn = row & 1023;
+  const float* Abase = accum + ((size_t)bb*8192 + nn)*64;
+  const __bf16* Wp = W + (size_t)(n0 + srow) * K + sk;
+  const float s3 = 1.0f/3.0f;
+  for (int k0 = 0; k0 < K; k0 += 32){
+    int c0 = k0 + sk;
+    const float* Ap = Abase + (size_t)(c0>>6)*65536 + (c0&63);
+    f32x4 a0=*(const f32x4*)(Ap), a1=*(const f32x4*)(Ap+4), a2=*(const f32x4*)(Ap+8), a3=*(const f32x4*)(Ap+12);
+    bf16x8 w0 = *(const bf16x8*)(Wp), w1 = *(const bf16x8*)(Wp+8);
+    Wp += 32;
+    __syncthreads();
+    bf16x8 va, vb;
+    #pragma unroll
+    for (int j=0;j<4;++j){ va[j]=(__bf16)(a0[j]*s3); va[j+4]=(__bf16)(a1[j]*s3);
+                           vb[j]=(__bf16)(a2[j]*s3); vb[j+4]=(__bf16)(a3[j]*s3); }
+    *(bf16x8*)&As[srow][sk]   = va;  *(bf16x8*)&As[srow][sk+8] = vb;
+    *(bf16x8*)&Ws[srow][sk]   = w0;  *(bf16x8*)&Ws[srow][sk+8] = w1;
+    __syncthreads();
+    bf16x8 aF[4], bF[4];
+    #pragma unroll
+    for (int mf=0;mf<4;++mf) aF[mf] = *(const bf16x8*)&As[wr*64+mf*16+lr][lg*8];
+    #pragma unroll
+    for (int nf=0;nf<4;++nf) bF[nf] = *(const bf16x8*)&Ws[wc*64+nf*16+lr][lg*8];
+    #pragma unroll
+    for (int mf=0;mf<4;++mf)
+      #pragma unroll
+      for (int nf=0;nf<4;++nf) acc[mf][nf] = MFMA(aF[mf], bF[nf], acc[mf][nf]);
+  }
+  #pragma unroll
+  for (int mf=0;mf<4;++mf)
+    #pragma unroll
+    for (int nf=0;nf<4;++nf){
+      int orow = m0 + wr*64 + mf*16 + lg*4;
+      int col = n0 + wc*64 + nf*16 + lr;
+      float bv = bias[col];
+      #pragma unroll
+      for (int r=0;r<4;++r) C[(size_t)(orow+r)*N + col] = acc[mf][nf][r] + bv;
+    }
 }
 
 extern "C" void kernel_launch(void* const* d_in, const int* in_sizes, int n_in,
@@ -867,30 +925,33 @@
   const float* mode_w = (const float*)d_in[36];
   float* ws  = (float*)d_ws;
   float* out = (float*)d_out;
-  __bf16* xb   = (__bf16*)(ws + OFF_XB);
-  __bf16* qwb  = (__bf16*)(ws + OFF_QW);
-  __bf16* mwb  = (__bf16*)(ws + OFF_MW2);
-  __bf16* wfb  = (__bf16*)(ws + OFF_WFB);
-  __bf16* pwb  = (__bf16*)(ws + OFF_PWB);
-  __bf16* qkvb = (__bf16*)(ws + OFF_R0);
+  __bf16* xb     = (__bf16*)(ws + OFF_XB);
+  __bf16* qwb    = (__bf16*)(ws + OFF_QW);
+  __bf16* mwb    = (__bf16*)(ws + OFF_MW2);
+  __bf16* wfb    = (__bf16*)(ws + OFF_WFB);
+  __bf16* pwb    = (__bf16*)(ws + OFF_PWB);
+  __bf16* qkvA   = (__bf16*)(ws + OFF_R0);
+  __bf16* qkvB   = qkvA + 12582912;
+  __bf16* gatesb = (__bf16*)out;
 
   k_const<<<1,256,0,stream>>>(ge_b1, ge_w2, ge_b2, mode_w, w5,b5,w7,b7,w9,b9,
                               pos_sw, neg_sw, spw, bih_f,bhh_f,bih_b,bhh_b, ws);
   k_cvt_all<<<3968,256,0,stream>>>(x, qkv_w, mha_in_w, wih_f, wih_b, proj_w, ws);
-  k_gemm_bf<float><<<512,256,0,stream>>>(xb, wfb, ws+OFF_LBIAS, ws+OFF_R0, 8, 1024, 512);
-  k_lstm_scan<<<16,256,0,stream>>>(whh_f, whh_b, ws+OFF_R0, ws+OFF_LC);
-  k_gemm_bf<__bf16><<<768,256,0,stream>>>(xb, mwb, mha_in_b, qkvb, 12, 1536, 512);
-  k_mha<1><<<dim3(4,4,8),256,0,stream>>>(qkvb, ws+OFF_ROWSUM, ws+OFF_COLW);
-  k_mha<2><<<dim3(4,4,8),256,0,stream>>>(qkvb, ws+OFF_ROWSUM, ws+OFF_COLW);
-  k_mha3<<<dim3(4,8,8),256,0,stream>>>(qkvb, ws+OFF_COLW, ws+OFF_ACMP);
-  k_xmean1<<<dim3(16,8),256,0,stream>>>(x, ws+OFF_XPART);
+  k_gemm_bf<<<512,256,0,stream>>>(xb, wfb, ws+OFF_LBIAS, gatesb, 8, 1024, 512);
+  k_mega1<<<912,256,0,stream>>>(whh_f, whh_b, gatesb, ws, x, xb, mwb, mha_in_b, qkvA);
+  k_gemm_bf<<<768,256,0,stream>>>(xb, qwb, nullptr, qkvB, 12, 1536, 512);
+  k_mega2<<<528,256,0,stream>>>(whh_f, whh_b, gatesb, ws, qkvA, qkvB, ws+OFF_ACCUM);
+  k_mha2_w<<<128,256,0,stream>>>(qkvA, ws+OFF_ROWSUM, ws+OFF_COLW);
+  k_mha3<<<dim3(4,8,8),256,0,stream>>>(qkvA, ws+OFF_COLW, ws+OFF_ACMP);
   k_coeffs<<<8,256,0,stream>>>(ws, mha_out_w, mha_out_b, ca_w1, ca_b1, ca_w2, ca_b2);
-  for (int s=0; s<3; ++s){
-    k_gemm_bf<__bf16><<<768,256,0,stream>>>(xb, qwb + (size_t)s*786432, nullptr, qkvb, 12, 1536, 512);
-    k_spec<<<dim3(2,8,8),256,0,stream>>>(qkvb, ws);
-    k_polar_kv<<<dim3(8,8),256,0,stream>>>(qkvb, ws, s);
-    k_polar_ap<<<dim3(8,8,8),256,0,stream>>>(qkvb, ws, ws+OFF_ACCUM, s);
-    k_conv<<<256,256,0,stream>>>(qkvb, ws, ws+OFF_ACCUM);
+  k_polar_kv<<<dim3(8,8),256,0,stream>>>(qkvB, ws, 0);
+  k_polar_ap<<<dim3(8,8,8),256,0,stream>>>(qkvB, ws, ws+OFF_ACCUM, 0);
+  for (int s=1; s<3; ++s){
+    k_gemm_bf<<<768,256,0,stream>>>(xb, qwb + (size_t)s*786432, nullptr, qkvB, 12, 1536, 512);
+    k_spec_w<<<128,256,0,stream>>>(qkvB, ws);
+    k_conv_w<<<256,256,0,stream>>>(qkvB, ws, ws+OFF_ACCUM);
+    k_polar_kv<<<dim3(8,8),256,0,stream>>>(qkvB, ws, s);
+    k_polar_ap<<<dim3(8,8,8),256,0,stream>>>(qkvB, ws, ws+OFF_ACCUM, s);
   }
   k_gemm_acc<<<256,256,0,stream>>>(ws+OFF_ACCUM, pwb, proj_b, out);
 }
```
